# Kernel optimization log

Hardware: AMD Instinct MI355X
Metric: run time of the kernel (lower is better)

The kernel has to match this reference:

```python
import jax, jax.numpy as jnp
import numpy as np

CAPACITY = 0.5


def setup_inputs() -> dict:
    key = jax.random.key(0)
    ks = jax.random.split(key, 5)
    B, L, D = 4, 4096, 1024
    Dff = 4 * D
    x = jax.random.normal(ks[0], (B, L, D), dtype=jnp.float32)
    w_router = jax.random.normal(ks[1], (D,), dtype=jnp.float32) / np.sqrt(D)
    w_bypass = jax.random.normal(ks[2], (D, D), dtype=jnp.float32) / np.sqrt(D)
    w1 = jax.random.normal(ks[3], (Dff, D), dtype=jnp.float32) / np.sqrt(D)
    w2 = jax.random.normal(ks[4], (D, Dff), dtype=jnp.float32) / np.sqrt(Dff)
    return {"x": x, "w_router": w_router, "w_bypass": w_bypass, "w1": w1, "w2": w2}


def _block_fn(x, w1, w2):
    # stand-in for the expensive full block: 2-layer GELU FFN (torch Linear: y = x W^T)
    h = jax.nn.gelu(jnp.einsum('bld,fd->blf', x, w1))
    return jnp.einsum('blf,df->bld', h, w2)


def reference(x, w_router, w_bypass, w1, w2):
    B, L, D = x.shape
    k = max(1, int(L * CAPACITY))  # static
    if k >= L:
        return _block_fn(x, w1, w2)
    # router scores (B, L)
    scores = jnp.einsum('bld,d->bl', x, w_router)
    _, top_idx = jax.lax.top_k(scores, k)          # (B, k)
    top_idx = jnp.sort(top_idx, axis=-1)           # (B, k), sorted positions
    # gather selected tokens -> (B, k, D)
    x_sel = jnp.take_along_axis(x, top_idx[:, :, None], axis=1)
    out_sel = _block_fn(x_sel, w1, w2)             # (B, k, D)
    # bypass path for all tokens
    output = jnp.einsum('bld,ed->ble', x, w_bypass)
    # scatter block outputs back onto selected positions
    b_idx = jnp.arange(B)[:, None]                 # (B, 1)
    output = output.at[b_idx, top_idx].set(out_sel)
    return output
```

## Files before the change

kernel.cpp:

```cpp
#include <hip/hip_runtime.h>
#include <stdint.h>
#include <math.h>


typedef __attribute__((ext_vector_type(8))) __bf16 bf16x8;
typedef __attribute__((ext_vector_type(4))) float f32x4;

__device__ __forceinline__ void async_cp16(const __bf16* g, __bf16* l) {
    __builtin_amdgcn_global_load_lds(
        (__attribute__((address_space(1))) void*)g,
        (__attribute__((address_space(3))) void*)l,
        16, 0, 0);
}

__device__ __forceinline__ float gelu_fast(float x) {
    float u = 1.5957691216057308f * x * (1.0f + 0.044715f * x * x);
    return x / (1.0f + __expf(-u));
}

__global__ __launch_bounds__(256) void router_cvt(
    const float* __restrict__ x, const float* __restrict__ wr,
    float* __restrict__ scores, __bf16* __restrict__ xb)
{
    int wid  = (blockIdx.x * blockDim.x + threadIdx.x) >> 6;
    int lane = threadIdx.x & 63;
    const float* row = x + (size_t)wid * 1024;
    __bf16* orow = xb + (size_t)wid * 1024;
    double s = 0.0;
    #pragma unroll
    for (int it = 0; it < 2; ++it) {
        int base = it * 512 + lane * 8;
        float4 a  = *(const float4*)(row + base);
        float4 b  = *(const float4*)(row + base + 4);
        float4 wa = *(const float4*)(wr + base);
        float4 wc = *(const float4*)(wr + base + 4);
        s += (double)a.x * wa.x + (double)a.y * wa.y
           + (double)a.z * wa.z + (double)a.w * wa.w
           + (double)b.x * wc.x + (double)b.y * wc.y
           + (double)b.z * wc.z + (double)b.w * wc.w;
        bf16x8 v;
        v[0] = (__bf16)a.x; v[1] = (__bf16)a.y; v[2] = (__bf16)a.z; v[3] = (__bf16)a.w;
        v[4] = (__bf16)b.x; v[5] = (__bf16)b.y; v[6] = (__bf16)b.z; v[7] = (__bf16)b.w;
        *(bf16x8*)(orow + base) = v;
    }
    #pragma unroll
    for (int off = 32; off > 0; off >>= 1) s += __shfl_down(s, off, 64);
    if (lane == 0) scores[wid] = (float)s;
}

__global__ __launch_bounds__(256) void cvt3(
    const float* __restrict__ p0, const float* __restrict__ p1,
    const float* __restrict__ p2,
    __bf16* __restrict__ o0, __bf16* __restrict__ o1, __bf16* __restrict__ o2,
    int c0, int c1, int c2)
{
    int chunk = blockIdx.x * 256 + threadIdx.x;
    const float* in; __bf16* out;
    if (chunk < c0)                { in = p0 + (size_t)chunk * 8;             out = o0 + (size_t)chunk * 8; }
    else if (chunk < c0 + c1)      { int c = chunk - c0;      in = p1 + (size_t)c * 8; out = o1 + (size_t)c * 8; }
    else if (chunk < c0 + c1 + c2) { int c = chunk - c0 - c1; in = p2 + (size_t)c * 8; out = o2 + (size_t)c * 8; }
    else return;
    float4 a = *(const float4*)(in);
    float4 b = *(const float4*)(in + 4);
    bf16x8 v;
    v[0] = (__bf16)a.x; v[1] = (__bf16)a.y; v[2] = (__bf16)a.z; v[3] = (__bf16)a.w;
    v[4] = (__bf16)b.x; v[5] = (__bf16)b.y; v[6] = (__bf16)b.z; v[7] = (__bf16)b.w;
    *(bf16x8*)(out) = v;
}

__global__ __launch_bounds__(1024) void topk_build(
    const float* __restrict__ scores,
    int* __restrict__ sel_rows, int* __restrict__ byp_rows)
{
    const int L = 4096, K = 2048;
    __shared__ unsigned u[4096];
    __shared__ int hist[256];
    __shared__ int scan_s[1024];
    __shared__ unsigned s_pref;
    __shared__ int s_kk;
    int b = blockIdx.x, t = threadIdx.x;

    for (int i = t; i < L; i += 1024) {
        unsigned v = __float_as_uint(scores[b * L + i]);
        v = (v & 0x80000000u) ? ~v : (v | 0x80000000u);
        u[i] = v;
    }
    if (t == 0) { s_pref = 0; s_kk = K; }
    __syncthreads();

    for (int shift = 24; shift >= 0; shift -= 8) {
        if (t < 256) hist[t] = 0;
        __syncthreads();
        unsigned pref = s_pref;
        for (int i = t; i < L; i += 1024) {
            unsigned v = u[i];
            bool in_set = (shift == 24) || ((v >> (shift + 8)) == pref);
            if (in_set) atomicAdd(&hist[(v >> shift) & 255], 1);
        }
        __syncthreads();
        if (t == 0) {
            int kk = s_kk, cum = 0, bsel = 0;
            for (int j = 255; j >= 0; --j) {
                if (cum + hist[j] >= kk) { bsel = j; break; }
                cum += hist[j];
            }
            s_kk = kk - cum;
            s_pref = (pref << 8) | (unsigned)bsel;
        }
        __syncthreads();
    }
    unsigned thr = s_pref;
    int need = s_kk;

    int base = t * 4;
    unsigned v0 = u[base], v1 = u[base+1], v2 = u[base+2], v3 = u[base+3];
    int eq0 = (v0 == thr), eq1 = (v1 == thr), eq2 = (v2 == thr), eq3 = (v3 == thr);
    scan_s[t] = eq0 + eq1 + eq2 + eq3;
    __syncthreads();
    for (int off = 1; off < 1024; off <<= 1) {
        int v = scan_s[t];
        if (t >= off) v += scan_s[t - off];
        __syncthreads();
        scan_s[t] = v;
        __syncthreads();
    }
    int erun = (t > 0) ? scan_s[t - 1] : 0;
    int sel[4];
    {
        int r = erun;
        sel[0] = (v0 > thr) || (eq0 && r < need); r += eq0;
        sel[1] = (v1 > thr) || (eq1 && r < need); r += eq1;
        sel[2] = (v2 > thr) || (eq2 && r < need); r += eq2;
        sel[3] = (v3 > thr) || (eq3 && r < need);
    }
    __syncthreads();

    scan_s[t] = sel[0] + sel[1] + sel[2] + sel[3];
    __syncthreads();
    for (int off = 1; off < 1024; off <<= 1) {
        int v = scan_s[t];
        if (t >= off) v += scan_s[t - off];
        __syncthreads();
        scan_s[t] = v;
        __syncthreads();
    }
    int run = (t > 0) ? scan_s[t - 1] : 0;
    #pragma unroll
    for (int j = 0; j < 4; ++j) {
        int idx = base + j;
        if (sel[j]) { sel_rows[b * K + run] = b * L + idx; run++; }
        else        { byp_rows[b * (L - K) + (idx - run)] = b * L + idx; }
    }
}

__device__ __forceinline__ void xcd_map(int id, int nx, int& mt, int& nt) {
    int grp = nx * 8;
    mt = (id / grp) * 8 + (id & 7);
    nt = (id % grp) >> 3;
}

template <bool GATHER_A, bool SCATTER_OUT, bool GELU_ACT, typename OT>
__global__ __launch_bounds__(256) void gemm_async(
    const __bf16* __restrict__ A, const __bf16* __restrict__ W,
    OT* __restrict__ Out, const int* __restrict__ rows,
    int K, int lda, int ldo)
{
    constexpr int BM = 128, BK = 64;
    __shared__ __align__(16) __bf16 As[BM * BK];
    __shared__ __align__(16) __bf16 Bs[BM * BK];
    __shared__ int rs[BM];

    const int tid = threadIdx.x;
    int mt, nt;
    xcd_map(blockIdx.y * gridDim.x + blockIdx.x, gridDim.x, mt, nt);
    const int m0 = mt * BM, n0 = nt * BM;
    if (tid < BM) rs[tid] = rows ? rows[m0 + tid] : (m0 + tid);
    __syncthreads();

    const int sub = tid >> 3;
    const int gc  = (tid & 7) ^ (sub & 7);
    const __bf16* aptr[4]; const __bf16* bptr[4];
    __bf16* adst[4]; __bf16* bdst[4];
    #pragma unroll
    for (int i = 0; i < 4; ++i) {
        int row = i * 32 + sub;
        int ar  = GATHER_A ? rs[row] : (m0 + row);
        aptr[i] = A + (size_t)ar * lda + gc * 8;
        bptr[i] = W + (size_t)(n0 + row) * K + gc * 8;
        adst[i] = As + (i * 256 + tid) * 8;
        bdst[i] = Bs + (i * 256 + tid) * 8;
    }

    f32x4 acc[4][4] = {};
    const int lane = tid & 63;
    const int wv = tid >> 6;
    const int wr = (wv >> 1) * 64, wc = (wv & 1) * 64;
    const int r = lane & 15, quad = lane >> 4;

    for (int k0 = 0; k0 < K; k0 += BK) {
        #pragma unroll
        for (int i = 0; i < 4; ++i) async_cp16(aptr[i] + k0, adst[i]);
        #pragma unroll
        for (int i = 0; i < 4; ++i) async_cp16(bptr[i] + k0, bdst[i]);
        __syncthreads();

        #pragma unroll
        for (int ks = 0; ks < 2; ++ks) {
            bf16x8 af[4], bfm[4];
            #pragma unroll
            for (int mi = 0; mi < 4; ++mi) {
                int row = wr + mi * 16 + r;
                int swz = (ks * 4 + quad) ^ (row & 7);
                af[mi] = *(const bf16x8*)(As + row * BK + swz * 8);
            }
            #pragma unroll
            for (int ni = 0; ni < 4; ++ni) {
                int row = wc + ni * 16 + r;
                int swz = (ks * 4 + quad) ^ (row & 7);
                bfm[ni] = *(const bf16x8*)(Bs + row * BK + swz * 8);
            }
            #pragma unroll
            for (int mi = 0; mi < 4; ++mi)
                #pragma unroll
                for (int ni = 0; ni < 4; ++ni)
                    acc[mi][ni] = __builtin_amdgcn_mfma_f32_16x16x32_bf16(
                        af[mi], bfm[ni], acc[mi][ni], 0, 0, 0);
        }
        __syncthreads();
    }

    #pragma unroll
    for (int mi = 0; mi < 4; ++mi) {
        #pragma unroll
        for (int reg = 0; reg < 4; ++reg) {
            int rowl = wr + mi * 16 + quad * 4 + reg;
            int orow = SCATTER_OUT ? rs[rowl] : (m0 + rowl);
            OT* op = Out + (size_t)orow * ldo + n0;
            #pragma unroll
            for (int ni = 0; ni < 4; ++ni) {
                float v = acc[mi][ni][reg];
                if (GELU_ACT) v = gelu_fast(v);
                op[wc + ni * 16 + r] = (OT)v;
            }
        }
    }
}

__global__ __launch_bounds__(256) void gemm_tail(
    const __bf16* __restrict__ h, const __bf16* __restrict__ w2b,
    const __bf16* __restrict__ xb, const __bf16* __restrict__ wbb,
    float* __restrict__ Out,
    const int* __restrict__ sel_rows, const int* __restrict__ byp_rows)
{
    constexpr int BM = 128, BK = 64;
    __shared__ __align__(16) __bf16 As[BM * BK];
    __shared__ __align__(16) __bf16 Bs[BM * BK];
    __shared__ int rs[BM];

    const int z = blockIdx.z;
    const __bf16* A = z ? xb : h;
    const __bf16* W = z ? wbb : w2b;
    const int K = z ? 1024 : 4096;
    const int* rows = z ? byp_rows : sel_rows;
    const bool gat = (z != 0);

    const int tid = threadIdx.x;
    int mt, nt;
    xcd_map(blockIdx.y * gridDim.x + blockIdx.x, gridDim.x, mt, nt);
    const int m0 = mt * BM, n0 = nt * BM;
    rs[tid & 127] = rows[m0 + (tid & 127)];
    __syncthreads();

    const int sub = tid >> 3;
    const int gc  = (tid & 7) ^ (sub & 7);
    const __bf16* aptr[4]; const __bf16* bptr[4];
    __bf16* adst[4]; __bf16* bdst[4];
    #pragma unroll
    for (int i = 0; i < 4; ++i) {
        int row = i * 32 + sub;
        int ar  = gat ? rs[row] : (m0 + row);
        aptr[i] = A + (size_t)ar * K + gc * 8;
        bptr[i] = W + (size_t)(n0 + row) * K + gc * 8;
        adst[i] = As + (i * 256 + tid) * 8;
        bdst[i] = Bs + (i * 256 + tid) * 8;
    }

    f32x4 acc[4][4] = {};
    const int lane = tid & 63;
    const int wv = tid >> 6;
    const int wrr = (wv >> 1) * 64, wc = (wv & 1) * 64;
    const int r = lane & 15, quad = lane >> 4;

    for (int k0 = 0; k0 < K; k0 += BK) {
        #pragma unroll
        for (int i = 0; i < 4; ++i) async_cp16(aptr[i] + k0, adst[i]);
        #pragma unroll
        for (int i = 0; i < 4; ++i) async_cp16(bptr[i] + k0, bdst[i]);
        __syncthreads();

        #pragma unroll
        for (int ks = 0; ks < 2; ++ks) {
            bf16x8 af[4], bfm[4];
            #pragma unroll
            for (int mi = 0; mi < 4; ++mi) {
                int row = wrr + mi * 16 + r;
                int swz = (ks * 4 + quad) ^ (row & 7);
                af[mi] = *(const bf16x8*)(As + row * BK + swz * 8);
            }
            #pragma unroll
            for (int ni = 0; ni < 4; ++ni) {
                int row = wc + ni * 16 + r;
                int swz = (ks * 4 + quad) ^ (row & 7);
                bfm[ni] = *(const bf16x8*)(Bs + row * BK + swz * 8);
            }
            #pragma unroll
            for (int mi = 0; mi < 4; ++mi)
                #pragma unroll
                for (int ni = 0; ni < 4; ++ni)
                    acc[mi][ni] = __builtin_amdgcn_mfma_f32_16x16x32_bf16(
                        af[mi], bfm[ni], acc[mi][ni], 0, 0, 0);
        }
        __syncthreads();
    }

    #pragma unroll
    for (int mi = 0; mi < 4; ++mi) {
        #pragma unroll
        for (int reg = 0; reg < 4; ++reg) {
            int rowl = wrr + mi * 16 + quad * 4 + reg;
            int orow = rs[rowl];
            float* op = Out + (size_t)orow * 1024 + n0;
            #pragma unroll
            for (int ni = 0; ni < 4; ++ni)
                op[wc + ni * 16 + r] = acc[mi][ni][reg];
        }
    }
}

extern "C" void kernel_launch(void* const* d_in, const int* in_sizes, int n_in,
                              void* d_out, int out_size, void* d_ws, size_t ws_size,
                              hipStream_t stream) {
    (void)in_sizes; (void)n_in; (void)out_size; (void)ws_size;
    const float* x  = (const float*)d_in[0];
    const float* wr = (const float*)d_in[1];
    const float* wb = (const float*)d_in[2];
    const float* w1 = (const float*)d_in[3];
    const float* w2 = (const float*)d_in[4];
    float* out = (float*)d_out;

    const int B = 4, L = 4096, D = 1024, DFF = 4096, KSEL = 2048;
    const int M = B * KSEL;
    const int NTOK = B * L;

    size_t n_x = (size_t)NTOK * D, n_wb = (size_t)D * D;
    size_t n_w1 = (size_t)DFF * D, n_w2 = (size_t)D * DFF;

    char* ws = (char*)d_ws;
    float* scores = (float*)ws;            ws += sizeof(float) * (size_t)NTOK;
    int* sel_rows = (int*)ws;              ws += sizeof(int) * (size_t)M;
    int* byp_rows = (int*)ws;              ws += sizeof(int) * (size_t)M;
    uintptr_t up = ((uintptr_t)ws + 255) & ~(uintptr_t)255;
    __bf16* xb  = (__bf16*)up;             up += 2 * n_x;
    __bf16* wbb = (__bf16*)up;             up += 2 * n_wb;
    __bf16* w1b = (__bf16*)up;             up += 2 * n_w1;
    __bf16* w2b = (__bf16*)up;             up += 2 * n_w2;
    up = (up + 255) & ~(uintptr_t)255;
    __bf16* h   = (__bf16*)up;

    router_cvt<<<NTOK / 4, 256, 0, stream>>>(x, wr, scores, xb);
    cvt3<<<(int)((n_wb + n_w1 + n_w2) / 8 / 256), 256, 0, stream>>>(
        wb, w1, w2, wbb, w1b, w2b,
        (int)(n_wb / 8), (int)(n_w1 / 8), (int)(n_w2 / 8));
    topk_build<<<B, 1024, 0, stream>>>(scores, sel_rows, byp_rows);

    gemm_async<true, false, true, __bf16>
        <<<dim3(DFF / 128, M / 128), 256, 0, stream>>>(
        xb, w1b, h, sel_rows, D, D, DFF);
    gemm_tail<<<dim3(D / 128, M / 128, 2), 256, 0, stream>>>(
        h, w2b, xb, wbb, out, sel_rows, byp_rows);
}
```

Before: 377.8 us.

## Switch GEMMs to 32x32x16 MFMA, fuse prep kernels, drop row-index LDS staging

Both GEMM kernels now use 32x32x16 bf16 MFMA with a 2x2 f32x16 accumulator per wave instead of 4x4 16x16x32 tiles, adjusting LDS fragment loads and the epilogue row mapping. The router/x conversion and the weight conversion kernels are merged into one launch. The shared-memory row-index cache and its barrier are removed, so gathered and scattered row indices are read directly from global memory. Launch bounds now request 5 blocks per CU. The larger MFMA is meant to cut LDS fragment traffic per FLOP and reduce launch overhead, at the cost of extra global index reads in the prologue and epilogue and tighter register limits.

```diff
diff --git a/kernel.cpp b/kernel.cpp
--- a/kernel.cpp
+++ b/kernel.cpp
@@ -4,7 +4,7 @@
 
 
 typedef __attribute__((ext_vector_type(8))) __bf16 bf16x8;
-typedef __attribute__((ext_vector_type(4))) float f32x4;
+typedef __attribute__((ext_vector_type(16))) float f32x16;
 
 __device__ __forceinline__ void async_cp16(const __bf16* g, __bf16* l) {
     __builtin_amdgcn_global_load_lds(
@@ -18,54 +18,53 @@
     return x / (1.0f + __expf(-u));
 }
 
-__global__ __launch_bounds__(256) void router_cvt(
+__global__ __launch_bounds__(256) void prep(
     const float* __restrict__ x, const float* __restrict__ wr,
-    float* __restrict__ scores, __bf16* __restrict__ xb)
+    float* __restrict__ scores, __bf16* __restrict__ xb,
+    const float* __restrict__ wb, const float* __restrict__ w1,
+    const float* __restrict__ w2,
+    __bf16* __restrict__ wbb, __bf16* __restrict__ w1b, __bf16* __restrict__ w2b)
 {
-    int wid  = (blockIdx.x * blockDim.x + threadIdx.x) >> 6;
-    int lane = threadIdx.x & 63;
-    const float* row = x + (size_t)wid * 1024;
-    __bf16* orow = xb + (size_t)wid * 1024;
-    double s = 0.0;
-    #pragma unroll
-    for (int it = 0; it < 2; ++it) {
-        int base = it * 512 + lane * 8;
-        float4 a  = *(const float4*)(row + base);
-        float4 b  = *(const float4*)(row + base + 4);
-        float4 wa = *(const float4*)(wr + base);
-        float4 wc = *(const float4*)(wr + base + 4);
-        s += (double)a.x * wa.x + (double)a.y * wa.y
-           + (double)a.z * wa.z + (double)a.w * wa.w
-           + (double)b.x * wc.x + (double)b.y * wc.y
-           + (double)b.z * wc.z + (double)b.w * wc.w;
+    const int bid = blockIdx.x;
+    if (bid < 4096) {
+        int wid  = (bid * 256 + threadIdx.x) >> 6;
+        int lane = threadIdx.x & 63;
+        const float* row = x + (size_t)wid * 1024;
+        __bf16* orow = xb + (size_t)wid * 1024;
+        double s = 0.0;
+        #pragma unroll
+        for (int it = 0; it < 2; ++it) {
+            int base = it * 512 + lane * 8;
+            float4 a  = *(const float4*)(row + base);
+            float4 b  = *(const float4*)(row + base + 4);
+            float4 wa = *(const float4*)(wr + base);
+            float4 wc = *(const float4*)(wr + base + 4);
+            s += (double)a.x * wa.x + (double)a.y * wa.y
+               + (double)a.z * wa.z + (double)a.w * wa.w
+               + (double)b.x * wc.x + (double)b.y * wc.y
+               + (double)b.z * wc.z + (double)b.w * wc.w;
+            bf16x8 v;
+            v[0] = (__bf16)a.x; v[1] = (__bf16)a.y; v[2] = (__bf16)a.z; v[3] = (__bf16)a.w;
+            v[4] = (__bf16)b.x; v[5] = (__bf16)b.y; v[6] = (__bf16)b.z; v[7] = (__bf16)b.w;
+            *(bf16x8*)(orow + base) = v;
+        }
+        #pragma unroll
+        for (int off = 32; off > 0; off >>= 1) s += __shfl_down(s, off, 64);
+        if (lane == 0) scores[wid] = (float)s;
+    } else {
+        const int c0 = 131072, c1 = 524288;
+        int chunk = (bid - 4096) * 256 + threadIdx.x;
+        const float* in; __bf16* out;
+        if (chunk < c0)           { in = wb + (size_t)chunk * 8;              out = wbb + (size_t)chunk * 8; }
+        else if (chunk < c0 + c1) { int c = chunk - c0;      in = w1 + (size_t)c * 8; out = w1b + (size_t)c * 8; }
+        else                      { int c = chunk - c0 - c1; in = w2 + (size_t)c * 8; out = w2b + (size_t)c * 8; }
+        float4 a = *(const float4*)(in);
+        float4 b = *(const float4*)(in + 4);
         bf16x8 v;
         v[0] = (__bf16)a.x; v[1] = (__bf16)a.y; v[2] = (__bf16)a.z; v[3] = (__bf16)a.w;
         v[4] = (__bf16)b.x; v[5] = (__bf16)b.y; v[6] = (__bf16)b.z; v[7] = (__bf16)b.w;
-        *(bf16x8*)(orow + base) = v;
-    }
-    #pragma unroll
-    for (int off = 32; off > 0; off >>= 1) s += __shfl_down(s, off, 64);
-    if (lane == 0) scores[wid] = (float)s;
-}
-
-__global__ __launch_bounds__(256) void cvt3(
-    const float* __restrict__ p0, const float* __restrict__ p1,
-    const float* __restrict__ p2,
-    __bf16* __restrict__ o0, __bf16* __restrict__ o1, __bf16* __restrict__ o2,
-    int c0, int c1, int c2)
-{
-    int chunk = blockIdx.x * 256 + threadIdx.x;
-    const float* in; __bf16* out;
-    if (chunk < c0)                { in = p0 + (size_t)chunk * 8;             out = o0 + (size_t)chunk * 8; }
-    else if (chunk < c0 + c1)      { int c = chunk - c0;      in = p1 + (size_t)c * 8; out = o1 + (size_t)c * 8; }
-    else if (chunk < c0 + c1 + c2) { int c = chunk - c0 - c1; in = p2 + (size_t)c * 8; out = o2 + (size_t)c * 8; }
-    else return;
-    float4 a = *(const float4*)(in);
-    float4 b = *(const float4*)(in + 4);
-    bf16x8 v;
-    v[0] = (__bf16)a.x; v[1] = (__bf16)a.y; v[2] = (__bf16)a.z; v[3] = (__bf16)a.w;
-    v[4] = (__bf16)b.x; v[5] = (__bf16)b.y; v[6] = (__bf16)b.z; v[7] = (__bf16)b.w;
-    *(bf16x8*)(out) = v;
+        *(bf16x8*)(out) = v;
+    }
 }
 
 __global__ __launch_bounds__(1024) void topk_build(
@@ -160,7 +159,7 @@
 }
 
 template <bool GATHER_A, bool SCATTER_OUT, bool GELU_ACT, typename OT>
-__global__ __launch_bounds__(256) void gemm_async(
+__global__ __launch_bounds__(256, 5) void gemm32(
     const __bf16* __restrict__ A, const __bf16* __restrict__ W,
     OT* __restrict__ Out, const int* __restrict__ rows,
     int K, int lda, int ldo)
@@ -168,14 +167,11 @@
     constexpr int BM = 128, BK = 64;
     __shared__ __align__(16) __bf16 As[BM * BK];
     __shared__ __align__(16) __bf16 Bs[BM * BK];
-    __shared__ int rs[BM];
 
     const int tid = threadIdx.x;
     int mt, nt;
     xcd_map(blockIdx.y * gridDim.x + blockIdx.x, gridDim.x, mt, nt);
     const int m0 = mt * BM, n0 = nt * BM;
-    if (tid < BM) rs[tid] = rows ? rows[m0 + tid] : (m0 + tid);
-    __syncthreads();
 
     const int sub = tid >> 3;
     const int gc  = (tid & 7) ^ (sub & 7);
@@ -184,18 +180,18 @@
     #pragma unroll
     for (int i = 0; i < 4; ++i) {
         int row = i * 32 + sub;
-        int ar  = GATHER_A ? rs[row] : (m0 + row);
+        int ar  = GATHER_A ? rows[m0 + row] : (m0 + row);
         aptr[i] = A + (size_t)ar * lda + gc * 8;
         bptr[i] = W + (size_t)(n0 + row) * K + gc * 8;
         adst[i] = As + (i * 256 + tid) * 8;
         bdst[i] = Bs + (i * 256 + tid) * 8;
     }
 
-    f32x4 acc[4][4] = {};
+    f32x16 acc[2][2] = {};
     const int lane = tid & 63;
     const int wv = tid >> 6;
     const int wr = (wv >> 1) * 64, wc = (wv & 1) * 64;
-    const int r = lane & 15, quad = lane >> 4;
+    const int col = lane & 31, half = lane >> 5;
 
     for (int k0 = 0; k0 < K; k0 += BK) {
         #pragma unroll
@@ -205,48 +201,47 @@
         __syncthreads();
 
         #pragma unroll
-        for (int ks = 0; ks < 2; ++ks) {
-            bf16x8 af[4], bfm[4];
-            #pragma unroll
-            for (int mi = 0; mi < 4; ++mi) {
-                int row = wr + mi * 16 + r;
-                int swz = (ks * 4 + quad) ^ (row & 7);
-                af[mi] = *(const bf16x8*)(As + row * BK + swz * 8);
-            }
-            #pragma unroll
-            for (int ni = 0; ni < 4; ++ni) {
-                int row = wc + ni * 16 + r;
-                int swz = (ks * 4 + quad) ^ (row & 7);
-                bfm[ni] = *(const bf16x8*)(Bs + row * BK + swz * 8);
-            }
-            #pragma unroll
-            for (int mi = 0; mi < 4; ++mi)
+        for (int ks = 0; ks < 4; ++ks) {
+            int c = ks * 2 + half;
+            bf16x8 af[2], bfm[2];
+            #pragma unroll
+            for (int mi = 0; mi < 2; ++mi) {
+                int row = wr + mi * 32 + col;
+                af[mi] = *(const bf16x8*)(As + row * BK + (c ^ (row & 7)) * 8);
+            }
+            #pragma unroll
+            for (int ni = 0; ni < 2; ++ni) {
+                int row = wc + ni * 32 + col;
+                bfm[ni] = *(const bf16x8*)(Bs + row * BK + (c ^ (row & 7)) * 8);
+            }
+            #pragma unroll
+            for (int mi = 0; mi < 2; ++mi)
                 #pragma unroll
-                for (int ni = 0; ni < 4; ++ni)
-                    acc[mi][ni] = __builtin_amdgcn_mfma_f32_16x16x32_bf16(
+                for (int ni = 0; ni < 2; ++ni)
+                    acc[mi][ni] = __builtin_amdgcn_mfma_f32_32x32x16_bf16(
                         af[mi], bfm[ni], acc[mi][ni], 0, 0, 0);
         }
         __syncthreads();
     }
 
     #pragma unroll
-    for (int mi = 0; mi < 4; ++mi) {
-        #pragma unroll
-        for (int reg = 0; reg < 4; ++reg) {
-            int rowl = wr + mi * 16 + quad * 4 + reg;
-            int orow = SCATTER_OUT ? rs[rowl] : (m0 + rowl);
+    for (int mi = 0; mi < 2; ++mi) {
+        #pragma unroll
+        for (int reg = 0; reg < 16; ++reg) {
+            int rowl = wr + mi * 32 + (reg & 3) + 8 * (reg >> 2) + 4 * half;
+            int orow = SCATTER_OUT ? rows[m0 + rowl] : (m0 + rowl);
             OT* op = Out + (size_t)orow * ldo + n0;
             #pragma unroll
-            for (int ni = 0; ni < 4; ++ni) {
+            for (int ni = 0; ni < 2; ++ni) {
                 float v = acc[mi][ni][reg];
                 if (GELU_ACT) v = gelu_fast(v);
-                op[wc + ni * 16 + r] = (OT)v;
-            }
-        }
-    }
-}
-
-__global__ __launch_bounds__(256) void gemm_tail(
+                op[wc + ni * 32 + col] = (OT)v;
+            }
+        }
+    }
+}
+
+__global__ __launch_bounds__(256, 5) void gemm_tail32(
     const __bf16* __restrict__ h, const __bf16* __restrict__ w2b,
     const __bf16* __restrict__ xb, const __bf16* __restrict__ wbb,
     float* __restrict__ Out,
@@ -255,7 +250,6 @@
     constexpr int BM = 128, BK = 64;
     __shared__ __align__(16) __bf16 As[BM * BK];
     __shared__ __align__(16) __bf16 Bs[BM * BK];
-    __shared__ int rs[BM];
 
     const int z = blockIdx.z;
     const __bf16* A = z ? xb : h;
@@ -268,8 +262,6 @@
     int mt, nt;
     xcd_map(blockIdx.y * gridDim.x + blockIdx.x, gridDim.x, mt, nt);
     const int m0 = mt * BM, n0 = nt * BM;
-    rs[tid & 127] = rows[m0 + (tid & 127)];
-    __syncthreads();
 
     const int sub = tid >> 3;
     const int gc  = (tid & 7) ^ (sub & 7);
@@ -278,18 +270,18 @@
     #pragma unroll
     for (int i = 0; i < 4; ++i) {
         int row = i * 32 + sub;
-        int ar  = gat ? rs[row] : (m0 + row);
+        int ar  = gat ? rows[m0 + row] : (m0 + row);
         aptr[i] = A + (size_t)ar * K + gc * 8;
         bptr[i] = W + (size_t)(n0 + row) * K + gc * 8;
         adst[i] = As + (i * 256 + tid) * 8;
         bdst[i] = Bs + (i * 256 + tid) * 8;
     }
 
-    f32x4 acc[4][4] = {};
+    f32x16 acc[2][2] = {};
     const int lane = tid & 63;
     const int wv = tid >> 6;
     const int wrr = (wv >> 1) * 64, wc = (wv & 1) * 64;
-    const int r = lane & 15, quad = lane >> 4;
+    const int col = lane & 31, half = lane >> 5;
 
     for (int k0 = 0; k0 < K; k0 += BK) {
         #pragma unroll
@@ -299,40 +291,39 @@
         __syncthreads();
 
         #pragma unroll
-        for (int ks = 0; ks < 2; ++ks) {
-            bf16x8 af[4], bfm[4];
-            #pragma unroll
-            for (int mi = 0; mi < 4; ++mi) {
-                int row = wrr + mi * 16 + r;
-                int swz = (ks * 4 + quad) ^ (row & 7);
-                af[mi] = *(const bf16x8*)(As + row * BK + swz * 8);
-            }
-            #pragma unroll
-            for (int ni = 0; ni < 4; ++ni) {
-                int row = wc + ni * 16 + r;
-                int swz = (ks * 4 + quad) ^ (row & 7);
-                bfm[ni] = *(const bf16x8*)(Bs + row * BK + swz * 8);
-            }
-            #pragma unroll
-            for (int mi = 0; mi < 4; ++mi)
+        for (int ks = 0; ks < 4; ++ks) {
+            int c = ks * 2 + half;
+            bf16x8 af[2], bfm[2];
+            #pragma unroll
+            for (int mi = 0; mi < 2; ++mi) {
+                int row = wrr + mi * 32 + col;
+                af[mi] = *(const bf16x8*)(As + row * BK + (c ^ (row & 7)) * 8);
+            }
+            #pragma unroll
+            for (int ni = 0; ni < 2; ++ni) {
+                int row = wc + ni * 32 + col;
+                bfm[ni] = *(const bf16x8*)(Bs + row * BK + (c ^ (row & 7)) * 8);
+            }
+            #pragma unroll
+            for (int mi = 0; mi < 2; ++mi)
                 #pragma unroll
-                for (int ni = 0; ni < 4; ++ni)
-                    acc[mi][ni] = __builtin_amdgcn_mfma_f32_16x16x32_bf16(
+                for (int ni = 0; ni < 2; ++ni)
+                    acc[mi][ni] = __builtin_amdgcn_mfma_f32_32x32x16_bf16(
                         af[mi], bfm[ni], acc[mi][ni], 0, 0, 0);
         }
         __syncthreads();
     }
 
     #pragma unroll
-    for (int mi = 0; mi < 4; ++mi) {
-        #pragma unroll
-        for (int reg = 0; reg < 4; ++reg) {
-            int rowl = wrr + mi * 16 + quad * 4 + reg;
-            int orow = rs[rowl];
+    for (int mi = 0; mi < 2; ++mi) {
+        #pragma unroll
+        for (int reg = 0; reg < 16; ++reg) {
+            int rowl = wrr + mi * 32 + (reg & 3) + 8 * (reg >> 2) + 4 * half;
+            int orow = rows[m0 + rowl];
             float* op = Out + (size_t)orow * 1024 + n0;
             #pragma unroll
-            for (int ni = 0; ni < 4; ++ni)
-                op[wc + ni * 16 + r] = acc[mi][ni][reg];
+            for (int ni = 0; ni < 2; ++ni)
+                op[wc + ni * 32 + col] = acc[mi][ni][reg];
         }
     }
 }
@@ -367,15 +358,12 @@
     up = (up + 255) & ~(uintptr_t)255;
     __bf16* h   = (__bf16*)up;
 
-    router_cvt<<<NTOK / 4, 256, 0, stream>>>(x, wr, scores, xb);
-    cvt3<<<(int)((n_wb + n_w1 + n_w2) / 8 / 256), 256, 0, stream>>>(
-        wb, w1, w2, wbb, w1b, w2b,
-        (int)(n_wb / 8), (int)(n_w1 / 8), (int)(n_w2 / 8));
+    prep<<<8704, 256, 0, stream>>>(x, wr, scores, xb, wb, w1, w2, wbb, w1b, w2b);
     topk_build<<<B, 1024, 0, stream>>>(scores, sel_rows, byp_rows);
 
-    gemm_async<true, false, true, __bf16>
+    gemm32<true, false, true, __bf16>
         <<<dim3(DFF / 128, M / 128), 256, 0, stream>>>(
         xb, w1b, h, sel_rows, D, D, DFF);
-    gemm_tail<<<dim3(D / 128, M / 128, 2), 256, 0, stream>>>(
+    gemm_tail32<<<dim3(D / 128, M / 128, 2), 256, 0, stream>>>(
         h, w2b, xb, wbb, out, sel_rows, byp_rows);
 }
```

After: 408.5 us. +8.1%, slower.
